# Kernel tuning notes

Measured on AMD Instinct MI355X. Metric: run time of the kernel, lower is better.

Reference implementation:

```python
import jax, jax.numpy as jnp
import numpy as np


def conv4d(x, w, b):
    """Valid 4D convolution.
    x: [B, Cin, T, D, H, W]; w: [Cout, Cin, kT, kD, kH, kW]; b: [Cout].
    Implemented as a fixed small loop over the kT kernel offsets, folding the
    output T positions into the batch of a 3D convolution (same math as the
    standard conv4d-via-conv3d decomposition used in torch).
    """
    B, Cin, T, D, H, W = x.shape
    Cout, _, kT, kD, kH, kW = w.shape
    To = T - kT + 1
    Do, Ho, Wo = D - kD + 1, H - kH + 1, W - kW + 1
    out = jnp.zeros((B * To, Cout, Do, Ho, Wo), dtype=x.dtype)
    for i in range(kT):  # kT in {3,4}: small fixed loop
        xs = jax.lax.slice_in_dim(x, i, i + To, axis=2)          # [B,Cin,To,D,H,W]
        xs = xs.transpose(0, 2, 1, 3, 4, 5).reshape(B * To, Cin, D, H, W)
        out = out + jax.lax.conv_general_dilated(
            xs, w[:, :, i], window_strides=(1, 1, 1), padding='VALID',
            dimension_numbers=('NCDHW', 'OIDHW', 'NCDHW'))
    out = out.reshape(B, To, Cout, Do, Ho, Wo).transpose(0, 2, 1, 3, 4, 5)
    return out + b[None, :, None, None, None, None]


def setup_inputs() -> dict:
    key = jax.random.key(0)
    ks = jax.random.split(key, 14)
    s = 0.1
    inp = {
        'x':  jax.random.normal(ks[0], (256, 1, 18, 18, 18, 18), dtype=jnp.float32),
        'w1': jax.random.normal(ks[1], (3, 1, 4, 4, 4, 4), dtype=jnp.float32) * s,
        'b1': jnp.zeros((3,), dtype=jnp.float32),
        'w2': jax.random.normal(ks[2], (3, 3, 4, 4, 4, 4), dtype=jnp.float32) * s,
        'b2': jnp.zeros((3,), dtype=jnp.float32),
        'w3': jax.random.normal(ks[3], (4, 3, 4, 4, 4, 4), dtype=jnp.float32) * s,
        'b3': jnp.zeros((4,), dtype=jnp.float32),
        'w4': jax.random.normal(ks[4], (5, 4, 4, 4, 4, 4), dtype=jnp.float32) * s,
        'b4': jnp.zeros((5,), dtype=jnp.float32),
        'w5': jax.random.normal(ks[5], (5, 5, 3, 3, 3, 3), dtype=jnp.float32) * s,
        'b5': jnp.zeros((5,), dtype=jnp.float32),
        'fc1_w': jax.random.normal(ks[6], (33, 1280), dtype=jnp.float32) * 0.02,
        'fc1_b': jnp.zeros((33,), dtype=jnp.float32),
        'fc2_w': jax.random.normal(ks[7], (1, 33), dtype=jnp.float32) * 0.02,
        'fc2_b': jnp.zeros((1,), dtype=jnp.float32),
    }
    return inp


def reference(x, w1, b1, w2, b2, w3, b3, w4, b4, w5, b5, fc1_w, fc1_b, fc2_w, fc2_b):
    h = jax.nn.relu(conv4d(x, w1, b1))
    h = jax.nn.relu(conv4d(h, w2, b2))
    h = jax.nn.relu(conv4d(h, w3, b3))
    h = jax.nn.relu(conv4d(h, w4, b4))
    h = jax.nn.relu(conv4d(h, w5, b5))   # [B, 5, 4, 4, 4, 4]
    h = h.reshape(h.shape[0], -1)        # [B, 1280]; Dropout is identity in eval
    h = jax.nn.relu(h @ fc1_w.T + fc1_b)
    return jax.nn.sigmoid(h @ fc2_w.T + fc2_b)  # [B, 1]
```

## Files before the change

### kernel.cpp

```cpp
#include <hip/hip_runtime.h>
#include <math.h>

#define BATCH 256
typedef unsigned int uint;
typedef unsigned short ushort;
typedef _Float16 half8 __attribute__((ext_vector_type(8)));
typedef float f32x4 __attribute__((ext_vector_type(4)));
typedef uint u32x4 __attribute__((ext_vector_type(4)));

#define GLOBAL_AS __attribute__((address_space(1)))
#define LDS_AS __attribute__((address_space(3)))

__device__ __forceinline__ ushort f2h(float f) {
  _Float16 h = (_Float16)f;
  return __builtin_bit_cast(ushort, h);
}
__device__ __forceinline__ float h2f(ushort u) {
  return (float)__builtin_bit_cast(_Float16, u);
}

template <int N>
__device__ __forceinline__ void waitv() {
  if constexpr (N == 0) {
    asm volatile("s_waitcnt vmcnt(0)" ::: "memory");
  } else if constexpr (N == 7) {
    asm volatile("s_waitcnt vmcnt(7)" ::: "memory");
  } else if constexpr (N == 9) {
    asm volatile("s_waitcnt vmcnt(9)" ::: "memory");
  } else if constexpr (N == 10) {
    asm volatile("s_waitcnt vmcnt(10)" ::: "memory");
  } else {
    static_assert(N == 0 || N == 7 || N == 9 || N == 10, "add literal");
  }
  __builtin_amdgcn_sched_barrier(0);
}

template <int NWG>
__device__ __forceinline__ int xcd_swz(int bid) {
  constexpr int Q = NWG / 8, R = NWG % 8;
  const int x = bid & 7, i = bid >> 3;
  return (x < R ? x * (Q + 1) : R * (Q + 1) + (x - R) * Q) + i;
}

__global__ __launch_bounds__(256) void transpose_kernel(
    const float* __restrict__ x, uint* __restrict__ xt) {
  __shared__ uint tile[65][65];
  const int P = 104976, NPP = 52488;
  const int pp0 = blockIdx.x * 64, b0 = blockIdx.y * 64;
  const int tx = threadIdx.x & 63, ty = threadIdx.x >> 6;
  for (int r = 0; r < 64; r += 4) {
    const int bl = ty + r, pp = pp0 + tx;
    if (pp < NPP) {
      const float2 v = *(const float2*)(x + (size_t)(b0 + bl) * P + 2 * pp);
      tile[tx][bl] = (uint)f2h(v.x) | ((uint)f2h(v.y) << 16);
    }
  }
  if (threadIdx.x < 64 && pp0 + 64 < NPP) {
    const int bl = threadIdx.x;
    const float2 v =
        *(const float2*)(x + (size_t)(b0 + bl) * P + 2 * (pp0 + 64));
    tile[64][bl] = (uint)f2h(v.x) | ((uint)f2h(v.y) << 16);
  }
  __syncthreads();
  for (int r = ty; r < 64; r += 4) {
    const int pp = pp0 + r;
    if (pp >= NPP) break;
    const int wp = pp % 9, sh = pp / 9;
    if (wp & 1) continue;
    uint2 o;
    o.x = tile[r][tx];
    o.y = (wp == 8) ? 0u : tile[r + 1][tx];
    *(uint2*)(xt + (size_t)(sh * 5 + (wp >> 1)) * 512 + (b0 + tx) * 2) = o;
  }
}

template <int CIN, int COUT, int KK, int S>
__global__ __launch_bounds__(256) void build_b(
    const float* __restrict__ w, ushort* __restrict__ Bg) {
  const int chunk = blockIdx.x;
  const int kd = chunk % KK, kt = (chunk / KK) % KK, ci = chunk / (KK * KK);
  for (int e = threadIdx.x; e < 512; e += 256) {
    int n = e >> 5, k = e & 31;
    int kh = k >> 3, wi = k & 7;
    int co = n / S, dw = n % S;
    int kw = wi - dw;
    float v = 0.f;
    if (co < COUT && kh < KK && kw >= 0 && kw < KK)
      v = w[((((co * CIN + ci) * KK + kt) * KK + kd) * KK + kh) * KK + kw];
    Bg[chunk * 512 + n * 32 + k] = f2h(v);
  }
}

template <int CIN, int COUT, int KK, int TI, int GIN, int GOUT, int HB,
          int PADSTART, int PADEND>
__global__ __launch_bounds__(256) void conv_wave(
    const ushort* __restrict__ xin, const ushort* __restrict__ Bg,
    const float* __restrict__ bias, ushort* __restrict__ out) {
  constexpr int S = 4;
  constexpr int WO = TI - KK + 1;
  constexpr int HTILES = WO / HB;
  constexpr int WTILES = (WO + S - 1) / S;
  constexpr int GX = HTILES * WTILES;
  constexpr int NWG = GX * WO * WO;
  constexpr int NC = CIN * KK * KK;
  static_assert(NC % 2 == 0, "pair-unrolled chunk loop needs even NC");
  constexpr int RS = 4 + HB - 1;
  constexpr int CH = RS + 1;
  constexpr int sH = GIN * 1024, sD = TI * sH, sT = TI * sD, sC = TI * sT;
  constexpr int oH = GOUT * 1024, oD = WO * oH, oT = WO * oD, oC = WO * oT;

  __shared__ ushort slab[4][2][RS * 512];

  const int wg = xcd_swz<NWG>(blockIdx.x);
  const int xb = wg % GX;
  const int d = (wg / GX) % WO;
  const int t = wg / (GX * WO);
  const int ht = xb % HTILES, wt = xb / HTILES;
  const int h0 = ht * HB, wb = wt * S;
  const int g0 = wb >> 2;

  const int tid = threadIdx.x;
  const int wave = tid >> 6, lane = tid & 63;
  const int quad = lane >> 4, mm = lane & 15;

  const int xsrc = (lane >> 5) * 1024 + wave * 256 + (lane & 31) * 8;
  const int bsrc = mm * 32 + quad * 8;

  f32x4 acc[HB][4];
#pragma unroll
  for (int dh = 0; dh < HB; dh++)
#pragma unroll
    for (int bt = 0; bt < 4; bt++) acc[dh][bt] = (f32x4){0.f, 0.f, 0.f, 0.f};

  auto stage = [&](int c, int buf) {
    const int kd = c % KK, kt2 = (c / KK) % KK, ci = c / (KK * KK);
    const ushort* base =
        xin + ci * sC + (t + kt2) * sT + (d + kd) * sD + h0 * sH + g0 * 1024;
    ushort* l = &slab[wave][buf][0];
#pragma unroll
    for (int r = 0; r < RS; r++)
      __builtin_amdgcn_global_load_lds(
          (const GLOBAL_AS uint*)(const void*)(base + r * sH + xsrc),
          (LDS_AS uint*)(void*)(l + r * 512), 16, 0, 0);
  };

  auto load_tf = [&](int c) -> u32x4 {
    return *(const u32x4*)(const void*)(Bg + c * 512 + bsrc);
  };

  auto compute = [&](int buf, u32x4 traw) {
    half8 tf = __builtin_bit_cast(half8, traw);
    const ushort* wsl = &slab[wave][buf][0];
#pragma unroll
    for (int dh = 0; dh < HB; dh++) {
      const ushort* arow = wsl + (dh + quad) * 512;
#pragma unroll
      for (int bt = 0; bt < 4; bt++) {
        const int bb = bt * 16 + mm;
        uint2 lo = *(const uint2*)(const void*)(arow + bb * 4);
        uint2 hi = *(const uint2*)(const void*)(arow + 256 + bb * 4);
        half8 xf = __builtin_bit_cast(half8, (u32x4){lo.x, lo.y, hi.x, hi.y});
        acc[dh][bt] =
            __builtin_amdgcn_mfma_f32_16x16x32_f16(tf, xf, acc[dh][bt], 0, 0, 0);
      }
    }
  };

  stage(0, 0);
  u32x4 tfA = load_tf(0);
  u32x4 tfB;

  for (int c = 0; c < NC; c += 2) {
    tfB = load_tf(c + 1);
    stage(c + 1, 1);
    waitv<CH>();
    compute(0, tfA);
    __builtin_amdgcn_sched_barrier(0);
    if (c + 2 < NC) {
      tfA = load_tf(c + 2);
      stage(c + 2, 0);
      waitv<CH>();
    } else {
      waitv<0>();
    }
    compute(1, tfB);
    __builtin_amdgcn_sched_barrier(0);
  }

  const bool is_last = (wb + S >= WO);
  const int co = quad;
#pragma unroll
  for (int dh = 0; dh < HB; dh++)
#pragma unroll
    for (int bt = 0; bt < 4; bt++) {
      const int b = wave * 64 + bt * 16 + mm;
      ushort* obase = out + t * oT + d * oD + (h0 + dh) * oH + b * 4;
      f32x4 v = acc[dh][bt];
      if (co < COUT) {
        const float bv = bias[co];
        float r0 = (wb + 0 < WO) ? fmaxf(v[0] + bv, 0.f) : 0.f;
        float r1 = (wb + 1 < WO) ? fmaxf(v[1] + bv, 0.f) : 0.f;
        float r2 = (wb + 2 < WO) ? fmaxf(v[2] + bv, 0.f) : 0.f;
        float r3 = (wb + 3 < WO) ? fmaxf(v[3] + bv, 0.f) : 0.f;
        uint2 pk;
        pk.x = (uint)f2h(r0) | ((uint)f2h(r1) << 16);
        pk.y = (uint)f2h(r2) | ((uint)f2h(r3) << 16);
        *(uint2*)(void*)(obase + co * oC + g0 * 1024) = pk;
        if constexpr (PADEND > PADSTART) {
          if (is_last) {
#pragma unroll
            for (int w = PADSTART; w < PADEND; w += 2)
              *(uint*)(void*)(obase + co * oC + (w >> 2) * 1024 + (w & 3)) = 0u;
          }
        }
      }
    }
}

template <int CIN, int COUT, int KK, int TI, int GIN, int GOUT, int S, int HB,
          int PADSTART, int PADEND>
__global__ __launch_bounds__(256) void conv_mfma(
    const ushort* __restrict__ xin, const ushort* __restrict__ Bg,
    const float* __restrict__ bias, ushort* __restrict__ out) {
  constexpr int WO = TI - KK + 1;
  constexpr int HTILES = WO / HB;
  constexpr int NC = CIN * KK * KK;
  constexpr int RS = 4 + HB - 1;
  constexpr int GW = (S == 4 ? 2 : 3);
  constexpr int ROWU = GW * 1024;
  constexpr int PROW = GW * 2;
  constexpr int sH = GIN * 1024, sD = TI * sH, sT = TI * sD, sC = TI * sT;
  constexpr int oH = GOUT * 1024, oD = WO * oH, oT = WO * oD, oC = WO * oT;

  __shared__ ushort slab[2][RS * ROWU];

  const int ht = blockIdx.x % HTILES;
  const int wt = blockIdx.x / HTILES;
  const int d = blockIdx.y, t = blockIdx.z;
  const int h0 = ht * HB, wb = wt * S;
  const int g0 = wb >> 2;

  const int tid = threadIdx.x;
  const int wave = tid >> 6, lane = tid & 63;
  const int quad = lane >> 4, mm = lane & 15;

  f32x4 acc[HB][4];
#pragma unroll
  for (int dh = 0; dh < HB; dh++)
#pragma unroll
    for (int bt = 0; bt < 4; bt++) acc[dh][bt] = (f32x4){0.f, 0.f, 0.f, 0.f};

  auto stage = [&](int c, int buf) {
    const int kd = c % KK, kt2 = (c / KK) % KK, ci = c / (KK * KK);
    const ushort* base =
        xin + ci * sC + (t + kt2) * sT + (d + kd) * sD + g0 * 1024;
    for (int r = wave; r < RS; r += 4) {
      int row = h0 + r;
      if (row > TI - 1) row = TI - 1;
      const ushort* g = base + row * sH;
      ushort* l = &slab[buf][r * ROWU];
#pragma unroll
      for (int p = 0; p < PROW; p++) {
        __builtin_amdgcn_global_load_lds(
            (const GLOBAL_AS uint*)(const void*)(g + p * 512 + lane * 8),
            (LDS_AS uint*)(void*)(l + p * 512), 16, 0, 0);
      }
    }
  };

  stage(0, 0);

  for (int c = 0; c < NC; c++) {
    __syncthreads();
    if (c + 1 < NC) stage(c + 1, (c + 1) & 1);

    u32x4 traw = *(const u32x4*)(const void*)(Bg + c * 512 + mm * 32 + quad * 8);
    half8 tf = __builtin_bit_cast(half8, traw);
    const int buf = c & 1;

#pragma unroll
    for (int dh = 0; dh < HB; dh++) {
      const ushort* arow = &slab[buf][(dh + quad) * ROWU];
#pragma unroll
      for (int bt = 0; bt < 4; bt++) {
        const int bidx = ((wave * 4 + bt) * 16 + mm) * 4;
        u32x4 raw;
        if ((wb & 2) == 0) {
          uint2 lo = *(const uint2*)(const void*)(arow + bidx);
          uint2 hi = *(const uint2*)(const void*)(arow + 1024 + bidx);
          raw = (u32x4){lo.x, lo.y, hi.x, hi.y};
        } else {
          uint c0 = *(const uint*)(const void*)(arow + bidx + 2);
          uint2 md = *(const uint2*)(const void*)(arow + 1024 + bidx);
          uint c1 = *(const uint*)(const void*)(arow + 2048 + bidx);
          raw = (u32x4){c0, md.x, md.y, c1};
        }
        half8 xf = __builtin_bit_cast(half8, raw);
        acc[dh][bt] =
            __builtin_amdgcn_mfma_f32_16x16x32_f16(tf, xf, acc[dh][bt], 0, 0, 0);
      }
    }
  }

  const bool is_last = (wb + S >= WO);
#pragma unroll
  for (int dh = 0; dh < HB; dh++)
#pragma unroll
    for (int bt = 0; bt < 4; bt++) {
      const int b = (wave * 4 + bt) * 16 + mm;
      ushort* obase = out + t * oT + d * oD + (h0 + dh) * oH + b * 4;
      f32x4 v = acc[dh][bt];
      const int co0 = quad * 2, co1 = co0 + 1;
      if (co0 < COUT) {
        const float bv = bias[co0];
        float r0 = fmaxf(v[0] + bv, 0.f), r1 = fmaxf(v[1] + bv, 0.f);
        *(uint*)(void*)(obase + co0 * oC + g0 * 1024 + (wb & 3)) =
            (uint)f2h(r0) | ((uint)f2h(r1) << 16);
      }
      if (co1 < COUT) {
        const float bv = bias[co1];
        float r2 = fmaxf(v[2] + bv, 0.f), r3 = fmaxf(v[3] + bv, 0.f);
        *(uint*)(void*)(obase + co1 * oC + g0 * 1024 + (wb & 3)) =
            (uint)f2h(r2) | ((uint)f2h(r3) << 16);
      }
      if constexpr (PADEND > PADSTART) {
        if (is_last) {
#pragma unroll
          for (int cc = 0; cc < 2; cc++) {
            const int co = quad * 2 + cc;
            if (co < COUT) {
#pragma unroll
              for (int w = PADSTART; w < PADEND; w += 2)
                *(uint*)(void*)(obase + co * oC + (w >> 2) * 1024 + (w & 3)) =
                    0u;
            }
          }
        }
      }
    }
}

__global__ __launch_bounds__(256) void fc1_kernel(
    const ushort* __restrict__ h, const float* __restrict__ w,
    const float* __restrict__ bias, float* __restrict__ out) {
  const int o = blockIdx.x, b = threadIdx.x;
  const float* wr = w + o * 1280;
  float a0 = 0.f, a1 = 0.f, a2 = 0.f, a3 = 0.f;
#pragma unroll 4
  for (int kq = 0; kq < 320; kq++) {
    const uint2 hv = *(const uint2*)(const void*)(h + (kq * 256 + b) * 4);
    a0 = fmaf(h2f((ushort)(hv.x & 0xffffu)), wr[4 * kq + 0], a0);
    a1 = fmaf(h2f((ushort)(hv.x >> 16)), wr[4 * kq + 1], a1);
    a2 = fmaf(h2f((ushort)(hv.y & 0xffffu)), wr[4 * kq + 2], a2);
    a3 = fmaf(h2f((ushort)(hv.y >> 16)), wr[4 * kq + 3], a3);
  }
  float acc = (a0 + a1) + (a2 + a3) + bias[o];
  out[o * BATCH + b] = acc > 0.f ? acc : 0.f;
}

__global__ __launch_bounds__(256) void fc2_kernel(
    const float* __restrict__ r, const float* __restrict__ w,
    const float* __restrict__ bias, float* __restrict__ out) {
  const int b = threadIdx.x;
  float acc = bias[0];
#pragma unroll
  for (int o = 0; o < 33; o++) acc = fmaf(r[o * BATCH + b], w[o], acc);
  out[b] = 1.f / (1.f + expf(-acc));
}

extern "C" void kernel_launch(void* const* d_in, const int* in_sizes, int n_in,
                              void* d_out, int out_size, void* d_ws,
                              size_t ws_size, hipStream_t stream) {
  const float* x    = (const float*)d_in[0];
  const float* w1   = (const float*)d_in[1];
  const float* b1   = (const float*)d_in[2];
  const float* w2   = (const float*)d_in[3];
  const float* b2   = (const float*)d_in[4];
  const float* w3   = (const float*)d_in[5];
  const float* b3   = (const float*)d_in[6];
  const float* w4   = (const float*)d_in[7];
  const float* b4   = (const float*)d_in[8];
  const float* w5   = (const float*)d_in[9];
  const float* b5   = (const float*)d_in[10];
  const float* fc1w = (const float*)d_in[11];
  const float* fc1b = (const float*)d_in[12];
  const float* fc2w = (const float*)d_in[13];
  const float* fc2b = (const float*)d_in[14];
  float* out = (float*)d_out;

  ushort* wsu = (ushort*)d_ws;
  ushort* R0 = wsu;
  ushort* R1 = wsu + 29900000;
  ushort* Bgb = wsu + 71400000;
  float* fo = (float*)(wsu + 71520000);

  ushort* xt = R0;
  ushort* h1 = R1;
  ushort* h2 = R0;
  ushort* h3 = R1;
  ushort* h4 = R0;
  ushort* h5 = R1;

  ushort* B1 = Bgb;
  ushort* B2 = Bgb + 16 * 512;
  ushort* B3 = Bgb + 64 * 512;
  ushort* B4 = Bgb + 112 * 512;
  ushort* B5 = Bgb + 176 * 512;

  build_b<1, 3, 4, 4><<<16, 256, 0, stream>>>(w1, B1);
  build_b<3, 3, 4, 4><<<48, 256, 0, stream>>>(w2, B2);
  build_b<3, 4, 4, 4><<<48, 256, 0, stream>>>(w3, B3);
  build_b<4, 5, 4, 2><<<64, 256, 0, stream>>>(w4, B4);
  build_b<5, 5, 3, 2><<<45, 256, 0, stream>>>(w5, B5);

  transpose_kernel<<<dim3(821, 4), 256, 0, stream>>>(x, (uint*)xt);

  conv_wave<1, 3, 4, 18, 5, 4, 3, 0, 0>
      <<<4500, 256, 0, stream>>>(xt, B1, b1, h1);
  conv_wave<3, 3, 4, 15, 4, 4, 3, 12, 16>
      <<<1728, 256, 0, stream>>>(h1, B2, b2, h2);
  conv_wave<3, 4, 4, 12, 4, 3, 3, 0, 0>
      <<<729, 256, 0, stream>>>(h2, B3, b3, h3);

  conv_mfma<4, 5, 4, 9, 3, 3, 2, 2, 6, 12>
      <<<dim3(9, 6, 6), 256, 0, stream>>>(h3, B4, b4, h4);
  conv_mfma<5, 5, 3, 6, 3, 1, 2, 2, 0, 0>
      <<<dim3(4, 4, 4), 256, 0, stream>>>(h4, B5, b5, h5);

  fc1_kernel<<<33, 256, 0, stream>>>(h5, fc1w, fc1b, fo);
  fc2_kernel<<<1, 256, 0, stream>>>(fo, fc2w, fc2b, out);
}
```

Measured before the change: 643.1 us.

## Split FC1 reduction across blocks and halve per-block work in tail convs

The fc1 kernel now splits its 1280-long reduction into 8 slices over a second grid dimension, writing partial sums that fc2 then combines with the fc1 bias and ReLU before the final dot product and sigmoid. The last two MFMA conv launches change a template parameter from 2 to 1 and double the grid's x dimension, presumably so each block handles less work. Both changes target the small tail kernels, which launch very few blocks and underfill the GPU. The cost is extra partial-sum traffic and a serial 8-way sum per output in fc2.

Result: faster. 580.3 us (-9.8%).

```diff
diff --git a/kernel.cpp b/kernel.cpp
--- a/kernel.cpp
+++ b/kernel.cpp
@@ -342,29 +342,35 @@
 
 __global__ __launch_bounds__(256) void fc1_kernel(
     const ushort* __restrict__ h, const float* __restrict__ w,
-    const float* __restrict__ bias, float* __restrict__ out) {
-  const int o = blockIdx.x, b = threadIdx.x;
-  const float* wr = w + o * 1280;
+    float* __restrict__ out) {
+  const int o = blockIdx.x, s = blockIdx.y, b = threadIdx.x;
+  const float* wr = w + o * 1280 + s * 160;
+  const ushort* hs = h + s * 40 * 1024;
   float a0 = 0.f, a1 = 0.f, a2 = 0.f, a3 = 0.f;
 #pragma unroll 4
-  for (int kq = 0; kq < 320; kq++) {
-    const uint2 hv = *(const uint2*)(const void*)(h + (kq * 256 + b) * 4);
+  for (int kq = 0; kq < 40; kq++) {
+    const uint2 hv = *(const uint2*)(const void*)(hs + kq * 1024 + b * 4);
     a0 = fmaf(h2f((ushort)(hv.x & 0xffffu)), wr[4 * kq + 0], a0);
     a1 = fmaf(h2f((ushort)(hv.x >> 16)), wr[4 * kq + 1], a1);
     a2 = fmaf(h2f((ushort)(hv.y & 0xffffu)), wr[4 * kq + 2], a2);
     a3 = fmaf(h2f((ushort)(hv.y >> 16)), wr[4 * kq + 3], a3);
   }
-  float acc = (a0 + a1) + (a2 + a3) + bias[o];
-  out[o * BATCH + b] = acc > 0.f ? acc : 0.f;
+  out[(s * 33 + o) * BATCH + b] = (a0 + a1) + (a2 + a3);
 }
 
 __global__ __launch_bounds__(256) void fc2_kernel(
-    const float* __restrict__ r, const float* __restrict__ w,
-    const float* __restrict__ bias, float* __restrict__ out) {
+    const float* __restrict__ r, const float* __restrict__ fc1b,
+    const float* __restrict__ w, const float* __restrict__ fc2b,
+    float* __restrict__ out) {
   const int b = threadIdx.x;
-  float acc = bias[0];
-#pragma unroll
-  for (int o = 0; o < 33; o++) acc = fmaf(r[o * BATCH + b], w[o], acc);
+  float acc = fc2b[0];
+#pragma unroll
+  for (int o = 0; o < 33; o++) {
+    float t = fc1b[o];
+#pragma unroll
+    for (int s = 0; s < 8; s++) t += r[(s * 33 + o) * BATCH + b];
+    acc = fmaf(t > 0.f ? t : 0.f, w[o], acc);
+  }
   out[b] = 1.f / (1.f + expf(-acc));
 }
 
@@ -422,11 +428,11 @@
   conv_wave<3, 4, 4, 12, 4, 3, 3, 0, 0>
       <<<729, 256, 0, stream>>>(h2, B3, b3, h3);
 
-  conv_mfma<4, 5, 4, 9, 3, 3, 2, 2, 6, 12>
-      <<<dim3(9, 6, 6), 256, 0, stream>>>(h3, B4, b4, h4);
-  conv_mfma<5, 5, 3, 6, 3, 1, 2, 2, 0, 0>
-      <<<dim3(4, 4, 4), 256, 0, stream>>>(h4, B5, b5, h5);
-
-  fc1_kernel<<<33, 256, 0, stream>>>(h5, fc1w, fc1b, fo);
-  fc2_kernel<<<1, 256, 0, stream>>>(fo, fc2w, fc2b, out);
-}
+  conv_mfma<4, 5, 4, 9, 3, 3, 2, 1, 6, 12>
+      <<<dim3(18, 6, 6), 256, 0, stream>>>(h3, B4, b4, h4);
+  conv_mfma<5, 5, 3, 6, 3, 1, 2, 1, 0, 0>
+      <<<dim3(8, 4, 4), 256, 0, stream>>>(h4, B5, b5, h5);
+
+  fc1_kernel<<<dim3(33, 8), 256, 0, stream>>>(h5, fc1w, fo);
+  fc2_kernel<<<1, 256, 0, stream>>>(fo, fc1b, fc2w, fc2b, out);
+}
```
